# Kernel tuning notes

Hardware: AMD Instinct MI355X
Metric: run time of the kernel (lower is better)

The kernel has to match this reference:

```python
import jax, jax.numpy as jnp
import numpy as np

B, S, D_IN, D, K, KU, L, M, H = 2, 1024, 64, 512, 16, 3, 2, 2, 2048
N_FFT = 2048  # next power of two >= 2*S - 1 (preconvolve padded_sl)
EPS = 1e-5


def setup_inputs() -> dict:
    key = jax.random.key(0)
    ks = jax.random.split(key, 8)
    # Hankel matrix Z[i,j] = 2 / ((i+j)^3 - (i+j)), i,j in 1..S; top-K eigh
    i = np.arange(1, S + 1, dtype=np.float64)
    s = i[:, None] + i[None, :]
    Z = 2.0 / (s ** 3 - s)
    evals, evecs = np.linalg.eigh(Z)
    sigma = jnp.asarray(evals[-K:], jnp.float32)          # (K,)
    phi = jnp.asarray(evecs[:, -K:], jnp.float32)         # (S, K)
    std = D ** -0.5
    return dict(
        inputs=jax.random.normal(ks[0], (B, S, D_IN), jnp.float32),
        sigma=sigma,
        phi=phi,
        in_proj_w=jax.random.normal(ks[1], (M, D, D_IN), jnp.float32) * (D_IN ** -0.5),
        rn_w=jnp.ones((M, L, D), jnp.float32),
        M_u=jax.random.uniform(ks[2], (M, L, KU, D, D), jnp.float32, -std, std),
        M_phi_plus=jax.random.normal(ks[3], (M, L, K, D, D), jnp.float32) * std,
        M_phi_minus=jax.random.normal(ks[4], (M, L, K, D, D), jnp.float32) * std,
        fc1_w=jax.random.normal(ks[5], (M, L, 2 * H, D), jnp.float32) * std,
        fc2_w=jax.random.normal(ks[6], (M, L, D, H), jnp.float32) * (H ** -0.5),
        out_proj_w=jax.random.normal(ks[7], (M, D_IN, D), jnp.float32) * std,
    )


def rmsnorm(x, w):
    return x * jax.lax.rsqrt(jnp.mean(x * x, axis=-1, keepdims=True) + EPS) * w


def compute_spectral(x, sigma, phi, mp, mm):
    # x: (B,S,D); phi: (S,K); mp/mm: (K,D,D)
    sgn = jnp.where(jnp.arange(S) % 2 == 0, 1.0, -1.0).astype(x.dtype)
    u2 = jnp.stack([x, x * sgn[None, :, None]], axis=-1)            # (B,S,D,2)
    U = jnp.fft.rfft(u2, n=N_FFT, axis=1)                           # (B,nf,D,2)
    Vf = jnp.fft.rfft(phi, n=N_FFT, axis=0)                         # (nf,K)
    Uc = jnp.fft.irfft(Vf[None, :, :, None, None] * U[:, :, None, :, :], n=N_FFT, axis=1)[:, :S]  # (B,S,K,D,2)
    Up = Uc[..., 0]
    Um = Uc[..., 1] * sgn[None, :, None, None]
    sig4 = sigma ** 0.25
    return (jnp.einsum('bskd,k,kdo->bso', Up, sig4, mp)
            + jnp.einsum('bskd,k,kdo->bso', Um, sig4, mm))


def compute_ar_u(mu, x):
    # y_t = sum_i x_{t-i} @ M_u[i]; mu: (KU,D,D)
    out = jnp.einsum('bsd,do->bso', x, mu[0])
    for i in range(1, KU):
        xi = jnp.pad(x[:, :S - i], ((0, 0), (i, 0), (0, 0)))
        out = out + jnp.einsum('bsd,do->bso', xi, mu[i])
    return out


def gated_mlp(x, w1, w2):
    y = x @ w1.T
    y, gate = jnp.split(y, 2, axis=-1)
    return (y * jax.nn.silu(gate)) @ w2.T


def reference(inputs, sigma, phi, in_proj_w, rn_w, M_u, M_phi_plus, M_phi_minus, fc1_w, fc2_w, out_proj_w):
    preds = jnp.zeros((B, S, D_IN), inputs.dtype)
    for m in range(M):  # ResidualSTU: sum of per-model predictions
        x = inputs @ in_proj_w[m].T
        for l in range(L):
            z = x
            h = rmsnorm(x, rn_w[m, l])
            spec = compute_spectral(h, sigma, phi, M_phi_plus[m, l], M_phi_minus[m, l])
            y_t = spec + compute_ar_u(M_u[m, l], h)  # use_ar_u=True, use_ar_y=False
            x = x + y_t
            x = x + gated_mlp(x, fc1_w[m, l], fc2_w[m, l])
            x = x + z
        preds = preds + x @ out_proj_w[m].T
    return preds
```

## Files before the change

kernel.cpp:

```cpp
#include <hip/hip_runtime.h>
#include <hip/hip_bf16.h>

typedef _Float16 f16;
typedef _Float16 half8 __attribute__((ext_vector_type(8)));
typedef float f32x4 __attribute__((ext_vector_type(4)));

#define S_LEN 1024
#define DMODEL 512
#define NFFT   2048
#define RPB    2048
#define RTOT   4096
#define CPS    1064
#define NROW   2048
#define NPART  4

__device__ __forceinline__ float2 mkf2(float a, float b) { float2 r; r.x = a; r.y = b; return r; }
__device__ __forceinline__ int zp(int i) { return i + (i >> 5); }
__device__ __forceinline__ float2 cmul(float2 w, float2 b) {
  return mkf2(b.x * w.x - b.y * w.y, b.x * w.y + b.y * w.x);
}
__device__ __forceinline__ float2 f2a(float2 a, float2 b) { return mkf2(a.x + b.x, a.y + b.y); }
__device__ __forceinline__ float2 f2s(float2 a, float2 b) { return mkf2(a.x - b.x, a.y - b.y); }

__device__ __forceinline__ void gl16(const f16* g, f16* l) {
  __builtin_amdgcn_global_load_lds((const __attribute__((address_space(1))) void*)g,
                                   (__attribute__((address_space(3))) void*)l, 16, 0, 0);
}

template<bool INV>
__device__ __forceinline__ void fft2048(float2* z, const float2* __restrict__ tw, int tid) {
  for (int i = tid; i < 2048; i += 256) {
    int j = (int)(__brev((unsigned)i) >> 21);
    if (i < j) { float2 a = z[zp(i)]; z[zp(i)] = z[zp(j)]; z[zp(j)] = a; }
  }
  __syncthreads();
#pragma unroll
  for (int r8 = 0; r8 < 3; ++r8) {
    const int sl = 1 + 3 * r8;
    const int h = 1 << (sl - 1);
    {
      int q = tid;
      int j = q & (h - 1);
      int i0 = ((q >> (sl - 1)) << (sl + 2)) + j;
      float2 a0 = z[zp(i0)],         a1 = z[zp(i0 + h)];
      float2 a2 = z[zp(i0 + 2 * h)], a3 = z[zp(i0 + 3 * h)];
      float2 a4 = z[zp(i0 + 4 * h)], a5 = z[zp(i0 + 5 * h)];
      float2 a6 = z[zp(i0 + 6 * h)], a7 = z[zp(i0 + 7 * h)];
      float2 wA  = tw[j << (11 - sl)];
      float2 wB0 = tw[j << (10 - sl)];
      float2 wB1 = tw[(j + h) << (10 - sl)];
      float2 wC0 = tw[j << (9 - sl)];
      float2 wC1 = tw[(j + h) << (9 - sl)];
      float2 wC2 = tw[(j + 2 * h) << (9 - sl)];
      float2 wC3 = tw[(j + 3 * h) << (9 - sl)];
      if (INV) {
        wA.y = -wA.y; wB0.y = -wB0.y; wB1.y = -wB1.y;
        wC0.y = -wC0.y; wC1.y = -wC1.y; wC2.y = -wC2.y; wC3.y = -wC3.y;
      }
      float2 t;
      t = cmul(wA, a1); float2 b0 = f2a(a0, t), b1 = f2s(a0, t);
      t = cmul(wA, a3); float2 b2 = f2a(a2, t), b3 = f2s(a2, t);
      t = cmul(wA, a5); float2 b4 = f2a(a4, t), b5 = f2s(a4, t);
      t = cmul(wA, a7); float2 b6 = f2a(a6, t), b7 = f2s(a6, t);
      t = cmul(wB0, b2); float2 c0 = f2a(b0, t), c2 = f2s(b0, t);
      t = cmul(wB1, b3); float2 c1 = f2a(b1, t), c3 = f2s(b1, t);
      t = cmul(wB0, b6); float2 c4 = f2a(b4, t), c6 = f2s(b4, t);
      t = cmul(wB1, b7); float2 c5 = f2a(b5, t), c7 = f2s(b5, t);
      t = cmul(wC0, c4); z[zp(i0)]         = f2a(c0, t); z[zp(i0 + 4 * h)] = f2s(c0, t);
      t = cmul(wC1, c5); z[zp(i0 + h)]     = f2a(c1, t); z[zp(i0 + 5 * h)] = f2s(c1, t);
      t = cmul(wC2, c6); z[zp(i0 + 2 * h)] = f2a(c2, t); z[zp(i0 + 6 * h)] = f2s(c2, t);
      t = cmul(wC3, c7); z[zp(i0 + 3 * h)] = f2a(c3, t); z[zp(i0 + 7 * h)] = f2s(c3, t);
    }
    __syncthreads();
  }
  for (int q = tid; q < 512; q += 256) {
    float2 a0 = z[zp(q)], a1 = z[zp(q + 512)], a2 = z[zp(q + 1024)], a3 = z[zp(q + 1536)];
    float2 w1 = tw[q << 1], w2 = tw[q], w3 = tw[q + 512];
    if (INV) { w1.y = -w1.y; w2.y = -w2.y; w3.y = -w3.y; }
    float2 t;
    t = cmul(w1, a1); float2 b0 = f2a(a0, t), b1 = f2s(a0, t);
    t = cmul(w1, a3); float2 b2 = f2a(a2, t), b3 = f2s(a2, t);
    t = cmul(w2, b2); z[zp(q)]        = f2a(b0, t); z[zp(q + 1024)] = f2s(b0, t);
    t = cmul(w3, b3); z[zp(q + 512)]  = f2a(b1, t); z[zp(q + 1536)] = f2s(b1, t);
  }
  __syncthreads();
}

__global__ void k_twiddle(float2* tw) {
  int i = blockIdx.x * 256 + threadIdx.x;
  if (i < 1024) {
    float ang = -6.2831853071795864769f * (float)i / 2048.0f;
    tw[i] = mkf2(cosf(ang), sinf(ang));
  }
}

__global__ void k_fft_phi(const float* __restrict__ phi, float2* __restrict__ Vf,
                          const float2* __restrict__ tw) {
  __shared__ float2 z[2112];
  int tid = threadIdx.x;
  int k0 = blockIdx.x * 2;
  for (int t = tid; t < 1024; t += 256)
    z[zp(t)] = *(const float2*)(phi + (size_t)t * 16 + k0);
  for (int t = 1024 + tid; t < 2048; t += 256) z[zp(t)] = mkf2(0.f, 0.f);
  __syncthreads();
  fft2048<false>(z, tw, tid);
  for (int f = tid; f <= 1024; f += 256) {
    float2 zf = z[zp(f)], zc = z[zp((2048 - f) & 2047)];
    Vf[(size_t)k0 * 1025 + f]       = mkf2(0.5f * (zf.x + zc.x), 0.5f * (zf.y - zc.y));
    Vf[(size_t)(k0 + 1) * 1025 + f] = mkf2(0.5f * (zf.y + zc.y), 0.5f * (zc.x - zf.x));
  }
}

__global__ void k_cpcm(const float2* __restrict__ Vf, const float* __restrict__ sigma,
                       float2* __restrict__ cpcm) {
  int idx = blockIdx.x * 256 + threadIdx.x;
  if (idx >= 32 * CPS) return;
  int kb = idx / CPS, f = idx - kb * CPS;
  int k = kb & 15;
  float s = powf(sigma[k], 0.25f) * (1.0f / 2048.0f);
  float2 v = mkf2(0.f, 0.f);
  if (f == 0) {
    float dc = Vf[(size_t)k * 1025].x;
    float ny = Vf[(size_t)k * 1025 + 1024].x;
    v = (kb < 16) ? mkf2(s * dc, s * ny) : mkf2(s * ny, s * dc);
  } else if (f <= 1023) {
    if (kb < 16) {
      v = Vf[(size_t)k * 1025 + f];
    } else {
      float2 t = Vf[(size_t)k * 1025 + (1024 - f)];
      v = mkf2(t.x, -t.y);
    }
    v.x *= s; v.y *= s;
  }
  cpcm[idx] = v;
}

__global__ __launch_bounds__(256)
void k_fwdcast(const f16* __restrict__ hb2, f16* __restrict__ Xbf,
               const float2* __restrict__ tw,
               const float* __restrict__ mp, const float* __restrict__ mm,
               const float* __restrict__ mu, const float* __restrict__ fc1,
               const float* __restrict__ fc2,
               f16* __restrict__ Wsp, f16* __restrict__ Wu,
               f16* __restrict__ Wf1, f16* __restrict__ Wf2) {
  __shared__ __align__(16) char smem[16896];
  int wg = (int)blockIdx.x, tid = threadIdx.x;
  if (wg < 512) {
    float2* z = (float2*)smem;
    int b = wg >> 8;
    int d0 = (wg & 255) * 2;
    for (int t = tid; t < 1024; t += 256) {
      union { unsigned v; f16 q[2]; } w;
      w.v = *(const unsigned*)(hb2 + (size_t)(b * 1026 + 2 + t) * 512 + d0);
      z[zp(t)] = mkf2((float)w.q[0], (float)w.q[1]);
    }
    for (int t = 1024 + tid; t < 2048; t += 256) z[zp(t)] = mkf2(0.f, 0.f);
    __syncthreads();
    fft2048<false>(z, tw, tid);
    for (int f = tid; f <= 1024; f += 256) {
      float2 zf = z[zp(f)], zc = z[zp((2048 - f) & 2047)];
      float x0r = 0.5f * (zf.x + zc.x), x0i = 0.5f * (zf.y - zc.y);
      float x1r = 0.5f * (zf.y + zc.y), x1i = 0.5f * (zc.x - zf.x);
      union { f16 h2[2]; unsigned u; } pr, pi;
      pr.h2[0] = (f16)x0r; pr.h2[1] = (f16)x1r;
      pi.h2[0] = (f16)x0i; pi.h2[1] = (f16)x1i;
      if (f == 0) {
        *(unsigned*)(Xbf + (size_t)(b * RPB) * 512 + d0) = pr.u;
      } else if (f == 1024) {
        *(unsigned*)(Xbf + (size_t)(b * RPB + 1) * 512 + d0) = pr.u;
      } else {
        *(unsigned*)(Xbf + (size_t)(b * RPB + 2 * f) * 512 + d0)     = pr.u;
        *(unsigned*)(Xbf + (size_t)(b * RPB + 2 * f + 1) * 512 + d0) = pi.u;
      }
    }
    return;
  }
  float* T = (float*)smem;
  int blk = wg - 512;
  if (blk < 2048) {
    int mat = blk >> 6, tile = blk & 63;
    int d0 = (tile >> 3) * 64, o0 = (tile & 7) * 64;
    const float* src = (mat < 16) ? (mp + (size_t)mat * 262144)
                                  : (mm + (size_t)(mat - 16) * 262144);
    for (int q = tid; q < 4096; q += 256) {
      int i = q >> 6, j = q & 63;
      T[i * 65 + j] = src[(size_t)(d0 + i) * 512 + o0 + j];
    }
    __syncthreads();
    for (int q = tid; q < 4096; q += 256) {
      int i = q >> 6, j = q & 63;
      Wsp[(size_t)(mat * 512 + o0 + i) * 512 + d0 + j] = (f16)T[j * 65 + i];
    }
  } else if (blk < 2240) {
    int q0 = blk - 2048;
    int ip = q0 >> 6, tile = q0 & 63;
    int d0 = (tile >> 3) * 64, o0 = (tile & 7) * 64;
    const float* src = mu + (size_t)(2 - ip) * 262144;
    for (int q = tid; q < 4096; q += 256) {
      int i = q >> 6, j = q & 63;
      T[i * 65 + j] = src[(size_t)(d0 + i) * 512 + o0 + j];
    }
    __syncthreads();
    for (int q = tid; q < 4096; q += 256) {
      int i = q >> 6, j = q & 63;
      Wu[(size_t)(o0 + i) * 1536 + ip * 512 + d0 + j] = (f16)T[j * 65 + i];
    }
  } else if (blk < 3264) {
    int q0 = blk - 2240;
    size_t e = ((size_t)q0 * 256 + tid) * 8;
    int jj = (int)(e >> 9), col = (int)(e & 511);
    int srow = (jj & 1) ? (2048 + (jj >> 1)) : (jj >> 1);
    const float4* s = (const float4*)(fc1 + (size_t)srow * 512 + col);
    float4 a = s[0], b = s[1];
    union { f16 h[8]; uint4 u; } pk;
    pk.h[0] = (f16)a.x; pk.h[1] = (f16)a.y; pk.h[2] = (f16)a.z; pk.h[3] = (f16)a.w;
    pk.h[4] = (f16)b.x; pk.h[5] = (f16)b.y; pk.h[6] = (f16)b.z; pk.h[7] = (f16)b.w;
    *(uint4*)(Wf1 + (size_t)jj * 512 + col) = pk.u;
  } else {
    int q0 = blk - 3264;
    size_t e = ((size_t)q0 * 256 + tid) * 8;
    const float4* s = (const float4*)(fc2 + e);
    float4 a = s[0], b = s[1];
    union { f16 h[8]; uint4 u; } pk;
    pk.h[0] = (f16)a.x; pk.h[1] = (f16)a.y; pk.h[2] = (f16)a.z; pk.h[3] = (f16)a.w;
    pk.h[4] = (f16)b.x; pk.h[5] = (f16)b.y; pk.h[6] = (f16)b.z; pk.h[7] = (f16)b.w;
    *(uint4*)(Wf2 + e) = pk.u;
  }
}

__global__ void k_rmsnorm(const f16* __restrict__ x, const float* __restrict__ w,
                          f16* __restrict__ hb2) {
  int tid = threadIdx.x, l = tid & 63, wv = tid >> 6;
  int r = blockIdx.x * 4 + wv;
  int b = r >> 10, t = r & 1023;
  const f16* xr = x + (size_t)r * 512;
  f16* hr = hb2 + (size_t)(b * 1026 + 2 + t) * 512;
  float v[8]; float ss = 0.f;
#pragma unroll
  for (int j = 0; j < 8; ++j) { v[j] = (float)xr[j * 64 + l]; ss += v[j] * v[j]; }
#pragma unroll
  for (int o = 32; o; o >>= 1) ss += __shfl_xor(ss, o, 64);
  float rn = rsqrtf(ss * (1.f / 512.f) + 1e-5f);
#pragma unroll
  for (int j = 0; j < 8; ++j) {
    float hv = v[j] * rn * w[j * 64 + l];
    hr[j * 64 + l] = (f16)hv;
  }
}

__global__ void k_fft_inv(const f16* __restrict__ P, f16* __restrict__ spec,
                          const float2* __restrict__ tw) {
  __shared__ float2 z[2112];
  int tid = threadIdx.x;
  int b = blockIdx.x >> 8;
  int o0 = (blockIdx.x & 255) * 2;
  for (int fp = tid; fp < 512; fp += 256) {
    int f0 = fp * 2;
    size_t base0 = (size_t)o0 * RTOT + (size_t)b * RPB + 2 * f0;
    float s0r[2] = {0.f, 0.f}, s0i[2] = {0.f, 0.f};
    float s1r[2] = {0.f, 0.f}, s1i[2] = {0.f, 0.f};
#pragma unroll
    for (int g = 0; g < NPART; ++g) {
      const f16* Pg = P + (size_t)g * 512 * RTOT;
      union { uint2 u; f16 h[4]; } ua, uc;
      ua.u = *(const uint2*)(Pg + base0);
      uc.u = *(const uint2*)(Pg + base0 + RTOT);
      s0r[0] += (float)ua.h[0]; s0i[0] += (float)ua.h[1];
      s0r[1] += (float)ua.h[2]; s0i[1] += (float)ua.h[3];
      s1r[0] += (float)uc.h[0]; s1i[0] += (float)uc.h[1];
      s1r[1] += (float)uc.h[2]; s1i[1] += (float)uc.h[3];
    }
    if (fp == 0) {
      z[zp(0)]    = mkf2(s0r[0], s1r[0]);
      z[zp(1024)] = mkf2(s0i[0], s1i[0]);
    } else {
      z[zp(f0)]        = mkf2(s0r[0] - s1i[0], s0i[0] + s1r[0]);
      z[zp(2048 - f0)] = mkf2(s0r[0] + s1i[0], s1r[0] - s0i[0]);
    }
    int f1 = f0 + 1;
    z[zp(f1)]        = mkf2(s0r[1] - s1i[1], s0i[1] + s1r[1]);
    z[zp(2048 - f1)] = mkf2(s0r[1] + s1i[1], s1r[1] - s0i[1]);
  }
  __syncthreads();
  fft2048<true>(z, tw, tid);
  for (int t = tid; t < 1024; t += 256) {
    float2 v = z[zp(t)];
    union { f16 h[2]; unsigned u; } pk;
    pk.h[0] = (f16)v.x; pk.h[1] = (f16)v.y;
    *(unsigned*)(spec + (size_t)(b * 1024 + t) * 512 + o0) = pk.u;
  }
}

__global__ __launch_bounds__(256, 2)
void k_gemm0(const f16* __restrict__ A, const f16* __restrict__ B0,
             const float* __restrict__ aux0, f16* __restrict__ outP) {
  __shared__ __align__(16) f16 As[128 * 128];
  __shared__ __align__(16) f16 Bs[128 * 128];
  const int tid = threadIdx.x, l = tid & 63, wvi = tid >> 6;
  const int wr = wvi >> 1, wc = wvi & 1;
  int wg = (int)blockIdx.x;
  wg = (wg & 7) * 64 + (wg >> 3);
  const int bz = wg >> 7; int rem = wg & 127;
  const int by = rem >> 2, bx = rem & 3;
  const int r0 = by * 128, c0 = bx * 128;

  f32x4 acc[4][4];
  f32x4 crun[4][4];
  f32x4 zz = {0.f, 0.f, 0.f, 0.f};
#pragma unroll
  for (int m = 0; m < 4; ++m)
#pragma unroll
    for (int n = 0; n < 4; ++n) { acc[m][n] = zz; crun[m][n] = zz; }

  const int rowl = tid >> 4;
  const int lc8 = ((tid & 15) ^ (rowl & 7)) * 8;
  f16* lA = As + ((tid >> 6) << 9);
  f16* lB = Bs + ((tid >> 6) << 9);
  const int lr = l & 15, kg = l >> 4, sw = l & 7;

  for (int s = 0; s < 32; ++s) {
    __syncthreads();
    {
      const int dblk = (s & 3) * 128;
      const int kb = bz * 8 + (s >> 2);
      const f16* Ab = A + (size_t)(r0 + rowl) * 512 + dblk + lc8;
      const f16* Bb = B0 + (size_t)(kb * 512 + c0 + rowl) * 512 + dblk + lc8;
#pragma unroll
      for (int i = 0; i < 8; ++i) {
        gl16(Ab + (size_t)i * 16 * 512, lA + i * 2048);
        gl16(Bb + (size_t)i * 16 * 512, lB + i * 2048);
      }
    }
    __syncthreads();
#pragma unroll
    for (int kk = 0; kk < 4; ++kk) {
      half8 af[4], bf[4];
      const int pc8 = (((kk * 4 + kg) ^ sw) << 3);
#pragma unroll
      for (int m = 0; m < 4; ++m)
        af[m] = *(const half8*)(As + (wr * 64 + m * 16 + lr) * 128 + pc8);
#pragma unroll
      for (int n = 0; n < 4; ++n)
        bf[n] = *(const half8*)(Bs + (wc * 64 + n * 16 + lr) * 128 + pc8);
#pragma unroll
      for (int m = 0; m < 4; ++m)
#pragma unroll
        for (int n = 0; n < 4; ++n)
          acc[m][n] = __builtin_amdgcn_mfma_f32_16x16x32_f16(af[m], bf[n], acc[m][n], 0, 0, 0);
    }
    if ((s & 3) == 3) {
      int kb = bz * 8 + (s >> 2);
#pragma unroll
      for (int m = 0; m < 4; ++m) {
        int R = r0 + wr * 64 + m * 16 + (kg << 2);
        int rb = R & (RPB - 1);
        bool dc = (rb == 0);
        float4 cs = *(const float4*)(aux0 + (size_t)kb * (CPS * 2) + (rb >> 1) * 2);
        float t1 = dc ? 0.f : cs.y;
        float t2 = dc ? cs.y : cs.x;
#pragma unroll
        for (int n = 0; n < 4; ++n) {
          f32x4 p = acc[m][n];
          crun[m][n].x += cs.x * p.x - t1 * p.y;
          crun[m][n].y += t2 * p.y + t1 * p.x;
          crun[m][n].z += cs.z * p.z - cs.w * p.w;
          crun[m][n].w += cs.z * p.w + cs.w * p.z;
          acc[m][n] = zz;
        }
      }
    }
  }

  f16* P = outP + (size_t)bz * (512ull * RTOT);
#pragma unroll
  for (int m = 0; m < 4; ++m) {
    int R0 = r0 + wr * 64 + m * 16 + (kg << 2);
#pragma unroll
    for (int n = 0; n < 4; ++n) {
      int o = c0 + wc * 64 + n * 16 + lr;
      union { f16 h[4]; uint2 u; } pk;
      pk.h[0] = (f16)crun[m][n].x; pk.h[1] = (f16)crun[m][n].y;
      pk.h[2] = (f16)crun[m][n].z; pk.h[3] = (f16)crun[m][n].w;
      *(uint2*)(P + (size_t)o * RTOT + R0) = pk.u;
    }
  }
}

template<int MODE, int MR, int NR>
__device__ __forceinline__ void stage(const f16* __restrict__ A, const f16* __restrict__ B0,
                                      int r0, int c0, int tid, int s,
                                      f16* As, f16* Bs) {
  constexpr int LDA = (MODE == 1) ? 1536 : (MODE == 2) ? 512 : 2048;
  const int kA = s * 64;
  const int rowl = tid >> 3;
  const int lc8 = ((tid & 7) ^ (rowl & 7)) * 8;
  f16* lA = As + ((tid >> 6) << 9);
  f16* lB = Bs + ((tid >> 6) << 9);
#pragma unroll
  for (int i = 0; i < MR; ++i) {
    int row = i * 32 + rowl;
    gl16(A + (size_t)(r0 + row) * LDA + kA + lc8, lA + i * 2048);
  }
#pragma unroll
  for (int i = 0; i < NR; ++i) {
    int row = i * 32 + rowl;
    const f16* bs;
    if constexpr (MODE == 1) {
      int ip = s >> 3, d0 = (s & 7) * 64;
      int rr = c0 + row;
      int b = rr >> 10, t = rr & 1023;
      bs = B0 + (size_t)(b * 1026 + t + ip) * 512 + d0 + lc8;
    } else {
      constexpr int LDB = (MODE == 2) ? 512 : 2048;
      bs = B0 + (size_t)(c0 + row) * LDB + s * 64 + lc8;
    }
    gl16(bs, lB + i * 2048);
  }
}

template<int MR, int NR>
__device__ __forceinline__ void mma_step(const f16* As, const f16* Bs, int l, int wr, int wc,
                                         f32x4 acc[MR][NR]) {
  const int lr = l & 15, kg = l >> 4, sw = l & 7;
#pragma unroll
  for (int kk = 0; kk < 2; ++kk) {
    half8 af[MR], bf[NR];
    const int pc8 = (((kk * 4 + kg) ^ sw) << 3);
#pragma unroll
    for (int m = 0; m < MR; ++m)
      af[m] = *(const half8*)(As + (wr * (MR * 16) + m * 16 + lr) * 64 + pc8);
#pragma unroll
    for (int n = 0; n < NR; ++n)
      bf[n] = *(const half8*)(Bs + (wc * (NR * 16) + n * 16 + lr) * 64 + pc8);
#pragma unroll
    for (int m = 0; m < MR; ++m)
#pragma unroll
      for (int n = 0; n < NR; ++n)
        acc[m][n] = __builtin_amdgcn_mfma_f32_16x16x32_f16(af[m], bf[n], acc[m][n], 0, 0, 0);
  }
}

template<int MODE, int MR, int NR>
__global__ __launch_bounds__(256, (MODE == 2) ? 3 : 4)
void k_gemm(const f16* __restrict__ A, const f16* __restrict__ B0,
            const f16* auxA, const f16* auxB, f16* __restrict__ outH) {
  __shared__ __align__(16) f16 As[MR * 32 * 64];
  __shared__ __align__(16) f16 Bs[NR * 32 * 64];
  const int tid = threadIdx.x, l = tid & 63, wvi = tid >> 6;
  const int wr = wvi >> 1, wc = wvi & 1;
  const int bx = blockIdx.x, by = blockIdx.y;
  const int r0 = by * (MR * 32), c0 = bx * (NR * 32);
  constexpr int KS = (MODE == 1) ? 24 : (MODE == 2) ? 8 : 32;

  f32x4 acc[MR][NR];
  f32x4 zz = {0.f, 0.f, 0.f, 0.f};
#pragma unroll
  for (int m = 0; m < MR; ++m)
#pragma unroll
    for (int n = 0; n < NR; ++n) acc[m][n] = zz;

  for (int s = 0; s < KS; ++s) {
    __syncthreads();
    stage<MODE, MR, NR>(A, B0, r0, c0, tid, s, As, Bs);
    __syncthreads();
    mma_step<MR, NR>(As, Bs, l, wr, wc, acc);
  }

  if constexpr (MODE == 1) {
#pragma unroll
    for (int m = 0; m < MR; ++m) {
      int o0 = r0 + wr * (MR * 16) + m * 16 + ((l >> 4) << 2);
#pragma unroll
      for (int n = 0; n < NR; ++n) {
        int r = c0 + wc * (NR * 16) + n * 16 + (l & 15);
        union { uint2 u; f16 h[4]; } xv, sv;
        xv.u = *(const uint2*)(auxA + (size_t)r * 512 + o0);
        sv.u = *(const uint2*)(auxB + (size_t)r * 512 + o0);
        f32x4 a = acc[m][n];
        union { f16 h[4]; uint2 u; } pk;
        pk.h[0] = (f16)((float)xv.h[0] + (float)sv.h[0] + a.x);
        pk.h[1] = (f16)((float)xv.h[1] + (float)sv.h[1] + a.y);
        pk.h[2] = (f16)((float)xv.h[2] + (float)sv.h[2] + a.z);
        pk.h[3] = (f16)((float)xv.h[3] + (float)sv.h[3] + a.w);
        *(uint2*)(outH + (size_t)r * 512 + o0) = pk.u;
      }
    }
  } else if constexpr (MODE == 2) {
#pragma unroll
    for (int m = 0; m < MR; ++m) {
      int jj0 = r0 + wr * (MR * 16) + m * 16 + ((l >> 4) << 2);
      int h2 = jj0 >> 1;
#pragma unroll
      for (int n = 0; n < NR; ++n) {
        int r = c0 + wc * (NR * 16) + n * 16 + (l & 15);
        f32x4 a = acc[m][n];
        float v0 = a.x * (a.y / (1.f + __expf(-a.y)));
        float v1 = a.z * (a.w / (1.f + __expf(-a.w)));
        union { f16 h[2]; unsigned u; } pk;
        pk.h[0] = (f16)v0; pk.h[1] = (f16)v1;
        *(unsigned*)(outH + (size_t)r * 2048 + h2) = pk.u;
      }
    }
  } else {
#pragma unroll
    for (int m = 0; m < MR; ++m) {
      int o0 = r0 + wr * (MR * 16) + m * 16 + ((l >> 4) << 2);
#pragma unroll
      for (int n = 0; n < NR; ++n) {
        int r = c0 + wc * (NR * 16) + n * 16 + (l & 15);
        union { uint2 u; f16 h[4]; } xv, x1v;
        xv.u  = *(const uint2*)(auxA + (size_t)r * 512 + o0);
        x1v.u = *(const uint2*)(auxB + (size_t)r * 512 + o0);
        f32x4 a = acc[m][n];
        union { f16 h[4]; uint2 u; } pk;
        pk.h[0] = (f16)((float)xv.h[0] + (float)x1v.h[0] + a.x);
        pk.h[1] = (f16)((float)xv.h[1] + (float)x1v.h[1] + a.y);
        pk.h[2] = (f16)((float)xv.h[2] + (float)x1v.h[2] + a.z);
        pk.h[3] = (f16)((float)xv.h[3] + (float)x1v.h[3] + a.w);
        *(uint2*)(outH + (size_t)r * 512 + o0) = pk.u;
      }
    }
  }
}

__global__ void k_inproj(const float* __restrict__ inp, const float* __restrict__ W,
                         f16* __restrict__ x) {
  __shared__ float row[64];
  int r = blockIdx.x, tid = threadIdx.x;
  if (tid < 64) row[tid] = inp[(size_t)r * 64 + tid];
  __syncthreads();
  for (int o = tid; o < 512; o += 256) {
    const float* wr = W + (size_t)o * 64;
    float acc = 0.f;
#pragma unroll 8
    for (int q = 0; q < 64; ++q) acc += row[q] * wr[q];
    x[(size_t)r * 512 + o] = (f16)acc;
  }
}

__global__ void k_outproj(const f16* __restrict__ x, const float* __restrict__ W,
                          float* out, int add) {
  __shared__ float row[512];
  int r = blockIdx.x, tid = threadIdx.x;
  for (int i = tid; i < 512; i += 256) row[i] = (float)x[(size_t)r * 512 + i];
  __syncthreads();
  int o = tid >> 2, part = tid & 3;
  const float* wr = W + (size_t)o * 512 + part * 128;
  const float* rp = row + part * 128;
  float acc = 0.f;
#pragma unroll 16
  for (int q = 0; q < 128; ++q) acc += rp[q] * wr[q];
  acc += __shfl_xor(acc, 1, 64);
  acc += __shfl_xor(acc, 2, 64);
  if (part == 0) {
    if (add) out[(size_t)r * 64 + o] += acc;
    else     out[(size_t)r * 64 + o] = acc;
  }
}

extern "C" void kernel_launch(void* const* d_in, const int* in_sizes, int n_in,
                              void* d_out, int out_size, void* d_ws, size_t ws_size,
                              hipStream_t stream) {
  const float* inputs    = (const float*)d_in[0];
  const float* sigma     = (const float*)d_in[1];
  const float* phi       = (const float*)d_in[2];
  const float* in_proj_w = (const float*)d_in[3];
  const float* rn_w      = (const float*)d_in[4];
  const float* M_u       = (const float*)d_in[5];
  const float* M_phi_p   = (const float*)d_in[6];
  const float* M_phi_m   = (const float*)d_in[7];
  const float* fc1       = (const float*)d_in[8];
  const float* fc2       = (const float*)d_in[9];
  const float* out_proj_w= (const float*)d_in[10];
  float* out = (float*)d_out;

  char* ws = (char*)d_ws;
  size_t off = 0;
  auto alloc = [&](size_t bytes) -> void* {
    void* p = ws + off;
    off += (bytes + 255) & ~(size_t)255;
    return p;
  };
  float2* tw   = (float2*)alloc(1024 * 8);
  float2* Vf   = (float2*)alloc((size_t)16 * 1025 * 8);
  float2* cpcm = (float2*)alloc((size_t)32 * CPS * 8);
  f16*    x    = (f16*)alloc((size_t)NROW * 512 * 2);
  f16*    hb2  = (f16*)alloc((size_t)2052 * 512 * 2);
  f16*    x1   = (f16*)alloc((size_t)NROW * 512 * 2);
  f16*    spec = (f16*)alloc((size_t)NROW * 512 * 2);
  f16*    Xbf  = (f16*)alloc((size_t)RTOT * 512 * 2);
  f16*    P    = (f16*)alloc((size_t)NPART * 512 * RTOT * 2);
  f16*    g1   = (f16*)alloc((size_t)NROW * 2048 * 2);
  f16*    Wsp  = (f16*)alloc((size_t)16384 * 512 * 2);
  f16*    Wu   = (f16*)alloc((size_t)512 * 1536 * 2);
  f16*    Wf1  = (f16*)alloc((size_t)4096 * 512 * 2);
  f16*    Wf2  = (f16*)alloc((size_t)512 * 2048 * 2);
  if (off > ws_size) return;

  hipMemsetAsync(hb2, 0, 2 * 512 * sizeof(f16), stream);
  hipMemsetAsync(hb2 + (size_t)1026 * 512, 0, 2 * 512 * sizeof(f16), stream);
  k_twiddle<<<4, 256, 0, stream>>>(tw);
  k_fft_phi<<<8, 256, 0, stream>>>(phi, Vf, tw);
  k_cpcm<<<133, 256, 0, stream>>>(Vf, sigma, cpcm);

  for (int m = 0; m < 2; ++m) {
    k_inproj<<<NROW, 256, 0, stream>>>(inputs, in_proj_w + (size_t)m * 512 * 64, x);
    for (int li = 0; li < 2; ++li) {
      int ml = m * 2 + li;
      k_rmsnorm<<<512, 256, 0, stream>>>(x, rn_w + (size_t)ml * 512, hb2);
      k_fwdcast<<<512 + 3776, 256, 0, stream>>>(
          hb2, Xbf, tw,
          M_phi_p + (size_t)ml * 16 * 262144, M_phi_m + (size_t)ml * 16 * 262144,
          M_u + (size_t)ml * 3 * 262144, fc1 + (size_t)ml * 4096 * 512,
          fc2 + (size_t)ml * 512 * 2048, Wsp, Wu, Wf1, Wf2);
      k_gemm0<<<dim3(512), 256, 0, stream>>>(Xbf, Wsp, (const float*)cpcm, P);
      k_fft_inv<<<512, 256, 0, stream>>>(P, spec, tw);
      k_gemm<1, 2, 2><<<dim3(32, 8), 256, 0, stream>>>(Wu, hb2, x, spec, x1);
      k_gemm<2, 4, 4><<<dim3(16, 32), 256, 0, stream>>>(Wf1, x1, nullptr, nullptr, g1);
      k_gemm<3, 2, 2><<<dim3(32, 8), 256, 0, stream>>>(Wf2, g1, x, x1, x);
    }
    k_outproj<<<NROW, 256, 0, stream>>>(x, out_proj_w + (size_t)m * 64 * 512, out, m);
  }
}
```

Baseline: 828.4 us.

## Batch both residual models into each kernel launch and halve gemm0 K-tile

Processes the two independent residual models together: every per-layer kernel gets a model index from its block id, and the workspace buffers are doubled so both models' activations and weights live side by side. This halves the number of launches and doubles grid sizes so the small kernels fill more of the GPU. The output projection now sums both models in one pass, so the read-modify-write of the output goes away. The spectral GEMM also moves from 128-wide to 64-wide K tiles, halving its shared memory at the cost of twice as many loop iterations and barriers.

```diff
diff --git a/kernel.cpp b/kernel.cpp
--- a/kernel.cpp
+++ b/kernel.cpp
@@ -137,21 +137,24 @@
 
 __global__ __launch_bounds__(256)
 void k_fwdcast(const f16* __restrict__ hb2, f16* __restrict__ Xbf,
-               const float2* __restrict__ tw,
-               const float* __restrict__ mp, const float* __restrict__ mm,
-               const float* __restrict__ mu, const float* __restrict__ fc1,
-               const float* __restrict__ fc2,
+               const float2* __restrict__ tw, int li,
+               const float* __restrict__ Mp, const float* __restrict__ Mm,
+               const float* __restrict__ Mu, const float* __restrict__ Fc1,
+               const float* __restrict__ Fc2,
                f16* __restrict__ Wsp, f16* __restrict__ Wu,
                f16* __restrict__ Wf1, f16* __restrict__ Wf2) {
   __shared__ __align__(16) char smem[16896];
   int wg = (int)blockIdx.x, tid = threadIdx.x;
-  if (wg < 512) {
+  if (wg < 1024) {
     float2* z = (float2*)smem;
-    int b = wg >> 8;
+    int model = wg >> 9;
+    int b = (wg >> 8) & 1;
     int d0 = (wg & 255) * 2;
+    const f16* hsrc = hb2 + (size_t)(model * 2 + b) * 1026 * 512;
+    f16* xdst = Xbf + (size_t)model * RTOT * 512 + (size_t)b * RPB * 512;
     for (int t = tid; t < 1024; t += 256) {
       union { unsigned v; f16 q[2]; } w;
-      w.v = *(const unsigned*)(hb2 + (size_t)(b * 1026 + 2 + t) * 512 + d0);
+      w.v = *(const unsigned*)(hsrc + (size_t)(2 + t) * 512 + d0);
       z[zp(t)] = mkf2((float)w.q[0], (float)w.q[1]);
     }
     for (int t = 1024 + tid; t < 2048; t += 256) z[zp(t)] = mkf2(0.f, 0.f);
@@ -165,18 +168,30 @@
       pr.h2[0] = (f16)x0r; pr.h2[1] = (f16)x1r;
       pi.h2[0] = (f16)x0i; pi.h2[1] = (f16)x1i;
       if (f == 0) {
-        *(unsigned*)(Xbf + (size_t)(b * RPB) * 512 + d0) = pr.u;
+        *(unsigned*)(xdst + d0) = pr.u;
       } else if (f == 1024) {
-        *(unsigned*)(Xbf + (size_t)(b * RPB + 1) * 512 + d0) = pr.u;
+        *(unsigned*)(xdst + (size_t)512 + d0) = pr.u;
       } else {
-        *(unsigned*)(Xbf + (size_t)(b * RPB + 2 * f) * 512 + d0)     = pr.u;
-        *(unsigned*)(Xbf + (size_t)(b * RPB + 2 * f + 1) * 512 + d0) = pi.u;
+        *(unsigned*)(xdst + (size_t)(2 * f) * 512 + d0)     = pr.u;
+        *(unsigned*)(xdst + (size_t)(2 * f + 1) * 512 + d0) = pi.u;
       }
     }
     return;
   }
   float* T = (float*)smem;
-  int blk = wg - 512;
+  int q0all = wg - 1024;
+  int model = q0all & 1;
+  int blk = q0all >> 1;
+  int ml = model * 2 + li;
+  const float* mp  = Mp  + (size_t)ml * 16 * 262144;
+  const float* mm  = Mm  + (size_t)ml * 16 * 262144;
+  const float* mu  = Mu  + (size_t)ml * 3 * 262144;
+  const float* fc1 = Fc1 + (size_t)ml * 4096 * 512;
+  const float* fc2 = Fc2 + (size_t)ml * 512 * 2048;
+  f16* WspM = Wsp + (size_t)model * 16384 * 512;
+  f16* WuM  = Wu  + (size_t)model * 512 * 1536;
+  f16* Wf1M = Wf1 + (size_t)model * 4096 * 512;
+  f16* Wf2M = Wf2 + (size_t)model * 512 * 2048;
   if (blk < 2048) {
     int mat = blk >> 6, tile = blk & 63;
     int d0 = (tile >> 3) * 64, o0 = (tile & 7) * 64;
@@ -189,11 +204,11 @@
     __syncthreads();
     for (int q = tid; q < 4096; q += 256) {
       int i = q >> 6, j = q & 63;
-      Wsp[(size_t)(mat * 512 + o0 + i) * 512 + d0 + j] = (f16)T[j * 65 + i];
+      WspM[(size_t)(mat * 512 + o0 + i) * 512 + d0 + j] = (f16)T[j * 65 + i];
     }
   } else if (blk < 2240) {
-    int q0 = blk - 2048;
-    int ip = q0 >> 6, tile = q0 & 63;
+    int q1 = blk - 2048;
+    int ip = q1 >> 6, tile = q1 & 63;
     int d0 = (tile >> 3) * 64, o0 = (tile & 7) * 64;
     const float* src = mu + (size_t)(2 - ip) * 262144;
     for (int q = tid; q < 4096; q += 256) {
@@ -203,11 +218,11 @@
     __syncthreads();
     for (int q = tid; q < 4096; q += 256) {
       int i = q >> 6, j = q & 63;
-      Wu[(size_t)(o0 + i) * 1536 + ip * 512 + d0 + j] = (f16)T[j * 65 + i];
+      WuM[(size_t)(o0 + i) * 1536 + ip * 512 + d0 + j] = (f16)T[j * 65 + i];
     }
   } else if (blk < 3264) {
-    int q0 = blk - 2240;
-    size_t e = ((size_t)q0 * 256 + tid) * 8;
+    int q1 = blk - 2240;
+    size_t e = ((size_t)q1 * 256 + tid) * 8;
     int jj = (int)(e >> 9), col = (int)(e & 511);
     int srow = (jj & 1) ? (2048 + (jj >> 1)) : (jj >> 1);
     const float4* s = (const float4*)(fc1 + (size_t)srow * 512 + col);
@@ -215,26 +230,29 @@
     union { f16 h[8]; uint4 u; } pk;
     pk.h[0] = (f16)a.x; pk.h[1] = (f16)a.y; pk.h[2] = (f16)a.z; pk.h[3] = (f16)a.w;
     pk.h[4] = (f16)b.x; pk.h[5] = (f16)b.y; pk.h[6] = (f16)b.z; pk.h[7] = (f16)b.w;
-    *(uint4*)(Wf1 + (size_t)jj * 512 + col) = pk.u;
+    *(uint4*)(Wf1M + (size_t)jj * 512 + col) = pk.u;
   } else {
-    int q0 = blk - 3264;
-    size_t e = ((size_t)q0 * 256 + tid) * 8;
+    int q1 = blk - 3264;
+    size_t e = ((size_t)q1 * 256 + tid) * 8;
     const float4* s = (const float4*)(fc2 + e);
     float4 a = s[0], b = s[1];
     union { f16 h[8]; uint4 u; } pk;
     pk.h[0] = (f16)a.x; pk.h[1] = (f16)a.y; pk.h[2] = (f16)a.z; pk.h[3] = (f16)a.w;
     pk.h[4] = (f16)b.x; pk.h[5] = (f16)b.y; pk.h[6] = (f16)b.z; pk.h[7] = (f16)b.w;
-    *(uint4*)(Wf2 + e) = pk.u;
-  }
-}
-
-__global__ void k_rmsnorm(const f16* __restrict__ x, const float* __restrict__ w,
+    *(uint4*)(Wf2M + e) = pk.u;
+  }
+}
+
+__global__ void k_rmsnorm(const f16* __restrict__ x, const float* __restrict__ rn_w, int li,
                           f16* __restrict__ hb2) {
   int tid = threadIdx.x, l = tid & 63, wv = tid >> 6;
   int r = blockIdx.x * 4 + wv;
-  int b = r >> 10, t = r & 1023;
+  int model = r >> 11;
+  int rl = r & 2047;
+  int b = rl >> 10, t = rl & 1023;
+  const float* w = rn_w + (size_t)(model * 2 + li) * 512;
   const f16* xr = x + (size_t)r * 512;
-  f16* hr = hb2 + (size_t)(b * 1026 + 2 + t) * 512;
+  f16* hr = hb2 + (size_t)((model * 2 + b) * 1026 + 2 + t) * 512;
   float v[8]; float ss = 0.f;
 #pragma unroll
   for (int j = 0; j < 8; ++j) { v[j] = (float)xr[j * 64 + l]; ss += v[j] * v[j]; }
@@ -252,8 +270,11 @@
                           const float2* __restrict__ tw) {
   __shared__ float2 z[2112];
   int tid = threadIdx.x;
-  int b = blockIdx.x >> 8;
-  int o0 = (blockIdx.x & 255) * 2;
+  int wg = (int)blockIdx.x;
+  int model = wg >> 9;
+  int b = (wg >> 8) & 1;
+  int o0 = (wg & 255) * 2;
+  const f16* Pm = P + (size_t)model * 512 * RTOT;
   for (int fp = tid; fp < 512; fp += 256) {
     int f0 = fp * 2;
     size_t base0 = (size_t)o0 * RTOT + (size_t)b * RPB + 2 * f0;
@@ -261,7 +282,7 @@
     float s1r[2] = {0.f, 0.f}, s1i[2] = {0.f, 0.f};
 #pragma unroll
     for (int g = 0; g < NPART; ++g) {
-      const f16* Pg = P + (size_t)g * 512 * RTOT;
+      const f16* Pg = Pm + (size_t)g * (2ull * 512 * RTOT);
       union { uint2 u; f16 h[4]; } ua, uc;
       ua.u = *(const uint2*)(Pg + base0);
       uc.u = *(const uint2*)(Pg + base0 + RTOT);
@@ -283,26 +304,31 @@
   }
   __syncthreads();
   fft2048<true>(z, tw, tid);
+  f16* sdst = spec + (size_t)(model * 2048 + b * 1024) * 512;
   for (int t = tid; t < 1024; t += 256) {
     float2 v = z[zp(t)];
     union { f16 h[2]; unsigned u; } pk;
     pk.h[0] = (f16)v.x; pk.h[1] = (f16)v.y;
-    *(unsigned*)(spec + (size_t)(b * 1024 + t) * 512 + o0) = pk.u;
+    *(unsigned*)(sdst + (size_t)t * 512 + o0) = pk.u;
   }
 }
 
 __global__ __launch_bounds__(256, 2)
-void k_gemm0(const f16* __restrict__ A, const f16* __restrict__ B0,
+void k_gemm0(const f16* __restrict__ A0, const f16* __restrict__ B00,
              const float* __restrict__ aux0, f16* __restrict__ outP) {
-  __shared__ __align__(16) f16 As[128 * 128];
-  __shared__ __align__(16) f16 Bs[128 * 128];
+  __shared__ __align__(16) f16 As[128 * 64];
+  __shared__ __align__(16) f16 Bs[128 * 64];
   const int tid = threadIdx.x, l = tid & 63, wvi = tid >> 6;
   const int wr = wvi >> 1, wc = wvi & 1;
   int wg = (int)blockIdx.x;
-  wg = (wg & 7) * 64 + (wg >> 3);
-  const int bz = wg >> 7; int rem = wg & 127;
+  wg = (wg & 7) * 128 + (wg >> 3);
+  const int model = wg >> 9;
+  int rem = wg & 511;
+  const int bz = rem >> 7; rem &= 127;
   const int by = rem >> 2, bx = rem & 3;
   const int r0 = by * 128, c0 = bx * 128;
+  const f16* A  = A0  + (size_t)model * RTOT * 512;
+  const f16* B0 = B00 + (size_t)model * 16384 * 512;
 
   f32x4 acc[4][4];
   f32x4 crun[4][4];
@@ -312,44 +338,42 @@
 #pragma unroll
     for (int n = 0; n < 4; ++n) { acc[m][n] = zz; crun[m][n] = zz; }
 
-  const int rowl = tid >> 4;
-  const int lc8 = ((tid & 15) ^ (rowl & 7)) * 8;
+  const int rowl = tid >> 3;
+  const int lc8 = ((tid & 7) ^ (rowl & 7)) * 8;
   f16* lA = As + ((tid >> 6) << 9);
   f16* lB = Bs + ((tid >> 6) << 9);
   const int lr = l & 15, kg = l >> 4, sw = l & 7;
 
-  for (int s = 0; s < 32; ++s) {
+  for (int s = 0; s < 64; ++s) {
     __syncthreads();
     {
-      const int dblk = (s & 3) * 128;
-      const int kb = bz * 8 + (s >> 2);
-      const f16* Ab = A + (size_t)(r0 + rowl) * 512 + dblk + lc8;
-      const f16* Bb = B0 + (size_t)(kb * 512 + c0 + rowl) * 512 + dblk + lc8;
-#pragma unroll
-      for (int i = 0; i < 8; ++i) {
-        gl16(Ab + (size_t)i * 16 * 512, lA + i * 2048);
-        gl16(Bb + (size_t)i * 16 * 512, lB + i * 2048);
+      const int kA = (s & 7) * 64;
+      const int kb = bz * 8 + (s >> 3);
+#pragma unroll
+      for (int i = 0; i < 4; ++i) {
+        gl16(A + (size_t)(r0 + i * 32 + rowl) * 512 + kA + lc8, lA + i * 2048);
+        gl16(B0 + (size_t)(kb * 512 + c0 + i * 32 + rowl) * 512 + kA + lc8, lB + i * 2048);
       }
     }
     __syncthreads();
 #pragma unroll
-    for (int kk = 0; kk < 4; ++kk) {
+    for (int kk = 0; kk < 2; ++kk) {
       half8 af[4], bf[4];
       const int pc8 = (((kk * 4 + kg) ^ sw) << 3);
 #pragma unroll
       for (int m = 0; m < 4; ++m)
-        af[m] = *(const half8*)(As + (wr * 64 + m * 16 + lr) * 128 + pc8);
+        af[m] = *(const half8*)(As + (wr * 64 + m * 16 + lr) * 64 + pc8);
 #pragma unroll
       for (int n = 0; n < 4; ++n)
-        bf[n] = *(const half8*)(Bs + (wc * 64 + n * 16 + lr) * 128 + pc8);
+        bf[n] = *(const half8*)(Bs + (wc * 64 + n * 16 + lr) * 64 + pc8);
 #pragma unroll
       for (int m = 0; m < 4; ++m)
 #pragma unroll
         for (int n = 0; n < 4; ++n)
           acc[m][n] = __builtin_amdgcn_mfma_f32_16x16x32_f16(af[m], bf[n], acc[m][n], 0, 0, 0);
     }
-    if ((s & 3) == 3) {
-      int kb = bz * 8 + (s >> 2);
+    if ((s & 7) == 7) {
+      int kb = bz * 8 + (s >> 3);
 #pragma unroll
       for (int m = 0; m < 4; ++m) {
         int R = r0 + wr * 64 + m * 16 + (kg << 2);
@@ -371,7 +395,7 @@
     }
   }
 
-  f16* P = outP + (size_t)bz * (512ull * RTOT);
+  f16* P = outP + (size_t)bz * (2ull * 512 * RTOT) + (size_t)model * 512 * RTOT;
 #pragma unroll
   for (int m = 0; m < 4; ++m) {
     int R0 = r0 + wr * 64 + m * 16 + (kg << 2);
@@ -442,15 +466,25 @@
 
 template<int MODE, int MR, int NR>
 __global__ __launch_bounds__(256, (MODE == 2) ? 3 : 4)
-void k_gemm(const f16* __restrict__ A, const f16* __restrict__ B0,
-            const f16* auxA, const f16* auxB, f16* __restrict__ outH) {
+void k_gemm(const f16* __restrict__ Ain, const f16* __restrict__ Bin,
+            const f16* auxAin, const f16* auxBin, f16* __restrict__ outIn) {
   __shared__ __align__(16) f16 As[MR * 32 * 64];
   __shared__ __align__(16) f16 Bs[NR * 32 * 64];
   const int tid = threadIdx.x, l = tid & 63, wvi = tid >> 6;
   const int wr = wvi >> 1, wc = wvi & 1;
-  const int bx = blockIdx.x, by = blockIdx.y;
+  const int bx = blockIdx.x, byi = blockIdx.y;
+  constexpr int BYD = (MODE == 2) ? 32 : 8;
+  const int model = byi / BYD, by = byi % BYD;
   const int r0 = by * (MR * 32), c0 = bx * (NR * 32);
   constexpr int KS = (MODE == 1) ? 24 : (MODE == 2) ? 8 : 32;
+  const size_t actOff = (size_t)model * 2048 * 512;
+  const f16* A = Ain + (size_t)model *
+      ((MODE == 1) ? 512ull * 1536 : (MODE == 2) ? 4096ull * 512 : 512ull * 2048);
+  const f16* B0 = Bin + ((MODE == 1) ? (size_t)model * 2 * 1026 * 512 :
+                         (MODE == 2) ? actOff : (size_t)model * 2048 * 2048);
+  const f16* auxA = auxAin + actOff;
+  const f16* auxB = auxBin + actOff;
+  f16* outH = outIn + ((MODE == 2) ? (size_t)model * 2048 * 2048 : actOff);
 
   f32x4 acc[MR][NR];
   f32x4 zz = {0.f, 0.f, 0.f, 0.f};
@@ -523,11 +557,13 @@
   }
 }
 
-__global__ void k_inproj(const float* __restrict__ inp, const float* __restrict__ W,
+__global__ void k_inproj(const float* __restrict__ inp, const float* __restrict__ Wall,
                          f16* __restrict__ x) {
   __shared__ float row[64];
   int r = blockIdx.x, tid = threadIdx.x;
-  if (tid < 64) row[tid] = inp[(size_t)r * 64 + tid];
+  int model = r >> 11, rl = r & 2047;
+  const float* W = Wall + (size_t)model * 512 * 64;
+  if (tid < 64) row[tid] = inp[(size_t)rl * 64 + tid];
   __syncthreads();
   for (int o = tid; o < 512; o += 256) {
     const float* wr = W + (size_t)o * 64;
@@ -538,24 +574,26 @@
   }
 }
 
-__global__ void k_outproj(const f16* __restrict__ x, const float* __restrict__ W,
-                          float* out, int add) {
-  __shared__ float row[512];
+__global__ void k_outproj(const f16* __restrict__ x, const float* __restrict__ Wall,
+                          float* out) {
+  __shared__ float row[1024];
   int r = blockIdx.x, tid = threadIdx.x;
-  for (int i = tid; i < 512; i += 256) row[i] = (float)x[(size_t)r * 512 + i];
+  for (int i = tid; i < 1024; i += 256) {
+    int mdl = i >> 9, c = i & 511;
+    row[i] = (float)x[((size_t)mdl * 2048 + r) * 512 + c];
+  }
   __syncthreads();
   int o = tid >> 2, part = tid & 3;
-  const float* wr = W + (size_t)o * 512 + part * 128;
-  const float* rp = row + part * 128;
+  const float* w0 = Wall + (size_t)o * 512 + part * 128;
+  const float* w1 = Wall + 64ull * 512 + (size_t)o * 512 + part * 128;
+  const float* r0 = row + part * 128;
+  const float* r1 = row + 512 + part * 128;
   float acc = 0.f;
 #pragma unroll 16
-  for (int q = 0; q < 128; ++q) acc += rp[q] * wr[q];
+  for (int q = 0; q < 128; ++q) acc += r0[q] * w0[q] + r1[q] * w1[q];
   acc += __shfl_xor(acc, 1, 64);
   acc += __shfl_xor(acc, 2, 64);
-  if (part == 0) {
-    if (add) out[(size_t)r * 64 + o] += acc;
-    else     out[(size_t)r * 64 + o] = acc;
-  }
+  if (part == 0) out[(size_t)r * 64 + o] = acc;
 }
 
 extern "C" void kernel_launch(void* const* d_in, const int* in_sizes, int n_in,
@@ -584,41 +622,35 @@
   float2* tw   = (float2*)alloc(1024 * 8);
   float2* Vf   = (float2*)alloc((size_t)16 * 1025 * 8);
   float2* cpcm = (float2*)alloc((size_t)32 * CPS * 8);
-  f16*    x    = (f16*)alloc((size_t)NROW * 512 * 2);
-  f16*    hb2  = (f16*)alloc((size_t)2052 * 512 * 2);
-  f16*    x1   = (f16*)alloc((size_t)NROW * 512 * 2);
-  f16*    spec = (f16*)alloc((size_t)NROW * 512 * 2);
-  f16*    Xbf  = (f16*)alloc((size_t)RTOT * 512 * 2);
-  f16*    P    = (f16*)alloc((size_t)NPART * 512 * RTOT * 2);
-  f16*    g1   = (f16*)alloc((size_t)NROW * 2048 * 2);
-  f16*    Wsp  = (f16*)alloc((size_t)16384 * 512 * 2);
-  f16*    Wu   = (f16*)alloc((size_t)512 * 1536 * 2);
-  f16*    Wf1  = (f16*)alloc((size_t)4096 * 512 * 2);
-  f16*    Wf2  = (f16*)alloc((size_t)512 * 2048 * 2);
+  f16*    x    = (f16*)alloc((size_t)2 * NROW * 512 * 2);
+  f16*    hb2  = (f16*)alloc((size_t)4 * 1026 * 512 * 2);
+  f16*    x1   = (f16*)alloc((size_t)2 * NROW * 512 * 2);
+  f16*    spec = (f16*)alloc((size_t)2 * NROW * 512 * 2);
+  f16*    Xbf  = (f16*)alloc((size_t)2 * RTOT * 512 * 2);
+  f16*    P    = (f16*)alloc((size_t)NPART * 2 * 512 * RTOT * 2);
+  f16*    g1   = (f16*)alloc((size_t)2 * NROW * 2048 * 2);
+  f16*    Wsp  = (f16*)alloc((size_t)2 * 16384 * 512 * 2);
+  f16*    Wu   = (f16*)alloc((size_t)2 * 512 * 1536 * 2);
+  f16*    Wf1  = (f16*)alloc((size_t)2 * 4096 * 512 * 2);
+  f16*    Wf2  = (f16*)alloc((size_t)2 * 512 * 2048 * 2);
   if (off > ws_size) return;
 
-  hipMemsetAsync(hb2, 0, 2 * 512 * sizeof(f16), stream);
-  hipMemsetAsync(hb2 + (size_t)1026 * 512, 0, 2 * 512 * sizeof(f16), stream);
+  for (int k = 0; k < 4; ++k)
+    hipMemsetAsync(hb2 + (size_t)k * 1026 * 512, 0, 2 * 512 * sizeof(f16), stream);
   k_twiddle<<<4, 256, 0, stream>>>(tw);
   k_fft_phi<<<8, 256, 0, stream>>>(phi, Vf, tw);
   k_cpcm<<<133, 256, 0, stream>>>(Vf, sigma, cpcm);
 
-  for (int m = 0; m < 2; ++m) {
-    k_inproj<<<NROW, 256, 0, stream>>>(inputs, in_proj_w + (size_t)m * 512 * 64, x);
-    for (int li = 0; li < 2; ++li) {
-      int ml = m * 2 + li;
-      k_rmsnorm<<<512, 256, 0, stream>>>(x, rn_w + (size_t)ml * 512, hb2);
-      k_fwdcast<<<512 + 3776, 256, 0, stream>>>(
-          hb2, Xbf, tw,
-          M_phi_p + (size_t)ml * 16 * 262144, M_phi_m + (size_t)ml * 16 * 262144,
-          M_u + (size_t)ml * 3 * 262144, fc1 + (size_t)ml * 4096 * 512,
-          fc2 + (size_t)ml * 512 * 2048, Wsp, Wu, Wf1, Wf2);
-      k_gemm0<<<dim3(512), 256, 0, stream>>>(Xbf, Wsp, (const float*)cpcm, P);
-      k_fft_inv<<<512, 256, 0, stream>>>(P, spec, tw);
-      k_gemm<1, 2, 2><<<dim3(32, 8), 256, 0, stream>>>(Wu, hb2, x, spec, x1);
-      k_gemm<2, 4, 4><<<dim3(16, 32), 256, 0, stream>>>(Wf1, x1, nullptr, nullptr, g1);
-      k_gemm<3, 2, 2><<<dim3(32, 8), 256, 0, stream>>>(Wf2, g1, x, x1, x);
-    }
-    k_outproj<<<NROW, 256, 0, stream>>>(x, out_proj_w + (size_t)m * 64 * 512, out, m);
-  }
-}
+  k_inproj<<<4096, 256, 0, stream>>>(inputs, in_proj_w, x);
+  for (int li = 0; li < 2; ++li) {
+    k_rmsnorm<<<1024, 256, 0, stream>>>(x, rn_w, li, hb2);
+    k_fwdcast<<<1024 + 7552, 256, 0, stream>>>(
+        hb2, Xbf, tw, li, M_phi_p, M_phi_m, M_u, fc1, fc2, Wsp, Wu, Wf1, Wf2);
+    k_gemm0<<<dim3(1024), 256, 0, stream>>>(Xbf, Wsp, (const float*)cpcm, P);
+    k_fft_inv<<<1024, 256, 0, stream>>>(P, spec, tw);
+    k_gemm<1, 2, 2><<<dim3(32, 16), 256, 0, stream>>>(Wu, hb2, x, spec, x1);
+    k_gemm<2, 4, 4><<<dim3(16, 64), 256, 0, stream>>>(Wf1, x1, nullptr, nullptr, g1);
+    k_gemm<3, 2, 2><<<dim3(32, 16), 256, 0, stream>>>(Wf2, g1, x, x1, x);
+  }
+  k_outproj<<<NROW, 256, 0, stream>>>(x, out_proj_w, out);
+}
```

After: 781.7 us. -5.6%, faster.
